# Performance work log

Hardware: AMD Instinct MI355X
Metric: run time of the kernel (lower is better)

## Reference

```python
import jax, jax.numpy as jnp
import numpy as np

NUM_HEADS = 16
HIDDEN = 1024
HEAD_DIM = HIDDEN // NUM_HEADS


def setup_inputs() -> dict:
    key = jax.random.key(0)
    ks = jax.random.split(key, 9)
    B, S = 2, 2048
    scale = 1.0 / np.sqrt(HIDDEN)
    x = jax.random.normal(ks[0], (B, S, HIDDEN), dtype=jnp.float32)
    Wq = jax.random.uniform(ks[1], (HIDDEN, HIDDEN), jnp.float32, -scale, scale)
    bq = jax.random.uniform(ks[2], (HIDDEN,), jnp.float32, -scale, scale)
    Wk = jax.random.uniform(ks[3], (HIDDEN, HIDDEN), jnp.float32, -scale, scale)
    bk = jax.random.uniform(ks[4], (HIDDEN,), jnp.float32, -scale, scale)
    Wv = jax.random.uniform(ks[5], (HIDDEN, HIDDEN), jnp.float32, -scale, scale)
    bv = jax.random.uniform(ks[6], (HIDDEN,), jnp.float32, -scale, scale)
    Wo = jax.random.uniform(ks[7], (HIDDEN, HIDDEN), jnp.float32, -scale, scale)
    bo = jax.random.uniform(ks[8], (HIDDEN,), jnp.float32, -scale, scale)
    return {"x": x, "Wq": Wq, "bq": bq, "Wk": Wk, "bk": bk,
            "Wv": Wv, "bv": bv, "Wo": Wo, "bo": bo}


def reference(x, Wq, bq, Wk, bk, Wv, bv, Wo, bo):
    B, S, _ = x.shape
    H, D = NUM_HEADS, HEAD_DIM
    # projections (torch Linear: x @ W^T + b)
    q = (x @ Wq.T + bq).reshape(B, S, H, D).transpose(0, 2, 1, 3)  # [B,H,S,D]
    k = (x @ Wk.T + bk).reshape(B, S, H, D).transpose(0, 2, 1, 3)
    v = (x @ Wv.T + bv).reshape(B, S, H, D).transpose(0, 2, 1, 3)
    scores = jnp.einsum("bhqd,bhkd->bhqk", q, k) / jnp.sqrt(jnp.float32(D))
    causal = jnp.tril(jnp.ones((S, S), dtype=bool))  # True = keep
    scores = jnp.where(causal, scores, -jnp.inf)
    weights = jax.nn.softmax(scores, axis=-1)
    out = jnp.einsum("bhqk,bhkd->bhqd", weights, v)  # [B,H,S,D]
    out = out.transpose(0, 2, 1, 3).reshape(B, S, H * D)
    return out @ Wo.T + bo
```

## Files before the change

### kernel.cpp

```cpp
#include <hip/hip_runtime.h>
#include <stdint.h>


#define HIDDEN 1024
#define NH 16
#define HD 64
#define BATCH 2
#define SEQ 2048

typedef unsigned short u16;
typedef unsigned int u32;
typedef __attribute__((ext_vector_type(8))) short short8;
typedef __attribute__((ext_vector_type(4))) float f32x4;

typedef const __attribute__((address_space(1))) u32 gu32;
typedef __attribute__((address_space(3))) u32 lu32;

__device__ __forceinline__ u16 f2bf(float f) {
    u32 u = __float_as_uint(f);
    return (u16)((u + 0x7FFFu + ((u >> 16) & 1u)) >> 16);
}

__global__ void cvt_all(const float* __restrict__ x, const float* __restrict__ Wq,
                        const float* __restrict__ Wk, const float* __restrict__ Wv,
                        const float* __restrict__ Wo, u16* __restrict__ xb,
                        u16* __restrict__ wqb, u16* __restrict__ wkb,
                        u16* __restrict__ wvb, u16* __restrict__ wob) {
    const int blk = blockIdx.x;
    const float* src; u16* dst; int base;
    if (blk < 2048)      { src = x;  dst = xb;  base = blk; }
    else if (blk < 2560) { src = Wq; dst = wqb; base = blk - 2048; }
    else if (blk < 3072) { src = Wk; dst = wkb; base = blk - 2560; }
    else if (blk < 3584) { src = Wv; dst = wvb; base = blk - 3072; }
    else                 { src = Wo; dst = wob; base = blk - 3584; }
    const int i = base * 256 + threadIdx.x;
    float4 a = ((const float4*)src)[2 * i];
    float4 b = ((const float4*)src)[2 * i + 1];
    union { u16 h[8]; uint4 v; } o;
    o.h[0] = f2bf(a.x); o.h[1] = f2bf(a.y); o.h[2] = f2bf(a.z); o.h[3] = f2bf(a.w);
    o.h[4] = f2bf(b.x); o.h[5] = f2bf(b.y); o.h[6] = f2bf(b.z); o.h[7] = f2bf(b.w);
    ((uint4*)dst)[i] = o.v;
}

#define GEMM_LDA 40
__device__ __forceinline__ void gemm_kloop(const u16* __restrict__ A,
                                           const u16* __restrict__ Wt,
                                           u16* As, u16* Bs, f32x4 (*acc)[4],
                                           int m0, int n0, int t) {
    const int lane = t & 63;
    const int w = t >> 6;
    const int quad = lane >> 4;
    const int lm = lane & 15;
    const int wm = (w & 1) * 64;
    const int wn = (w >> 1) * 64;
    const int srow = t >> 2;
    const int schunk = (t & 3) * 8;
    for (int k0 = 0; k0 < 1024; k0 += 32) {
        uint4 a0 = *(const uint4*)(A + (size_t)(m0 + srow) * 1024 + k0 + schunk);
        uint4 a1 = *(const uint4*)(A + (size_t)(m0 + srow + 64) * 1024 + k0 + schunk);
        uint4 b0 = *(const uint4*)(Wt + (size_t)(n0 + srow) * 1024 + k0 + schunk);
        uint4 b1 = *(const uint4*)(Wt + (size_t)(n0 + srow + 64) * 1024 + k0 + schunk);
        __syncthreads();
        *(uint4*)(As + srow * GEMM_LDA + schunk) = a0;
        *(uint4*)(As + (srow + 64) * GEMM_LDA + schunk) = a1;
        *(uint4*)(Bs + srow * GEMM_LDA + schunk) = b0;
        *(uint4*)(Bs + (srow + 64) * GEMM_LDA + schunk) = b1;
        __syncthreads();
        short8 af[4], bf[4];
#pragma unroll
        for (int mi = 0; mi < 4; mi++)
            af[mi] = *(const short8*)(As + (wm + mi * 16 + lm) * GEMM_LDA + quad * 8);
#pragma unroll
        for (int ni = 0; ni < 4; ni++)
            bf[ni] = *(const short8*)(Bs + (wn + ni * 16 + lm) * GEMM_LDA + quad * 8);
#pragma unroll
        for (int mi = 0; mi < 4; mi++)
#pragma unroll
            for (int ni = 0; ni < 4; ni++)
                acc[mi][ni] = __builtin_amdgcn_mfma_f32_16x16x32_bf16(
                    af[mi], bf[ni], acc[mi][ni], 0, 0, 0);
    }
}

__launch_bounds__(256, 2)
__global__ void gemm_qkv(const u16* __restrict__ A, const u16* __restrict__ Wqb,
                         const u16* __restrict__ Wkb, const u16* __restrict__ Wvb,
                         const float* __restrict__ bq, const float* __restrict__ bk,
                         const float* __restrict__ bv, u16* __restrict__ Qo,
                         u16* __restrict__ Ko, u16* __restrict__ Vo) {
    __shared__ u16 As[128 * GEMM_LDA];
    __shared__ u16 Bs[128 * GEMM_LDA];
    const int which = blockIdx.x >> 3;
    const int n0 = (blockIdx.x & 7) * 128;
    const int m0 = blockIdx.y * 128;
    const u16* Wt = (which == 0) ? Wqb : (which == 1) ? Wkb : Wvb;
    const float* bias = (which == 0) ? bq : (which == 1) ? bk : bv;
    u16* out = (which == 0) ? Qo : (which == 1) ? Ko : Vo;
    const float oscale = (which == 0) ? 0.18033688011112042f : 1.0f;
    const int t = threadIdx.x;
    const int lane = t & 63, w = t >> 6, quad = lane >> 4, lm = lane & 15;
    const int wm = (w & 1) * 64, wn = (w >> 1) * 64;

    f32x4 acc[4][4] = {};
    gemm_kloop(A, Wt, As, Bs, acc, m0, n0, t);

#pragma unroll
    for (int ni = 0; ni < 4; ni++) {
        const int n = n0 + wn + ni * 16 + lm;
        const float bv_ = bias[n];
        const int h = n >> 6, d = n & 63;
#pragma unroll
        for (int mi = 0; mi < 4; mi++)
#pragma unroll
            for (int r = 0; r < 4; r++) {
                const int m = m0 + wm + mi * 16 + quad * 4 + r;
                const int b = m >> 11, s = m & 2047;
                const u16 hv = f2bf((acc[mi][ni][r] + bv_) * oscale);
                if (which == 2)
                    out[(((size_t)(b * NH + h) * HD + d) * SEQ) + s] = hv;
                else
                    out[(((size_t)(b * NH + h) * SEQ + s) * HD) + d] = hv;
            }
    }
}

__launch_bounds__(256, 2)
__global__ void gemm_out(const u16* __restrict__ A, const u16* __restrict__ Wt,
                         const float* __restrict__ bias, float* __restrict__ out) {
    __shared__ u16 As[128 * GEMM_LDA];
    __shared__ u16 Bs[128 * GEMM_LDA];
    const int n0 = blockIdx.x * 128;
    const int m0 = blockIdx.y * 128;
    const int t = threadIdx.x;
    const int lane = t & 63, w = t >> 6, quad = lane >> 4, lm = lane & 15;
    const int wm = (w & 1) * 64, wn = (w >> 1) * 64;

    f32x4 acc[4][4] = {};
    gemm_kloop(A, Wt, As, Bs, acc, m0, n0, t);

#pragma unroll
    for (int ni = 0; ni < 4; ni++) {
        const int n = n0 + wn + ni * 16 + lm;
        const float bv_ = bias[n];
#pragma unroll
        for (int mi = 0; mi < 4; mi++)
#pragma unroll
            for (int r = 0; r < 4; r++) {
                const int m = m0 + wm + mi * 16 + quad * 4 + r;
                out[(size_t)m * 1024 + n] = acc[mi][ni][r] + bv_;
            }
    }
}

__launch_bounds__(256, 3)
__global__ void attn_kernel(const u16* __restrict__ Q, const u16* __restrict__ K,
                            const u16* __restrict__ Vt, u16* __restrict__ Out) {
    constexpr int LDP = 68;
    __shared__ u16 Ks[2][64 * 64];
    __shared__ u16 Vs[2][64 * 64];
    __shared__ u16 Ps[4 * 16 * LDP];
    const int t = threadIdx.x;
    const int lane = t & 63, w = t >> 6, quad = lane >> 4, lm = lane & 15;
    const int qt = 31 - (blockIdx.x >> 5);
    const int bh = blockIdx.x & 31;
    const int b = bh >> 4, h = bh & 15;
    const size_t base = (size_t)(b * NH + h) * SEQ * HD;
    const u16* Qg = Q + base;
    const u16* Kg = K + base;
    const u16* Vg = Vt + base;
    const int q0 = qt * 64 + w * 16;
    const int nk = qt + 1;

    short8 qf[2];
#pragma unroll
    for (int kk = 0; kk < 2; kk++)
        qf[kk] = *(const short8*)(Qg + (size_t)(q0 + lm) * HD + kk * 32 + quad * 8);

    f32x4 oacc[4] = {};
    f32x4 lacc = {};
    short8 ones;
#pragma unroll
    for (int j = 0; j < 8; j++) ones[j] = (short)0x3F80;

    u16* Pw = Ps + w * 16 * LDP;

    const int srow = (lane >> 3);
    const int schunk = (lane & 7) ^ srow;
    auto stage_kv = [&](int kt, int buf) {
#pragma unroll
        for (int j = 0; j < 2; j++) {
            const int row = w * 16 + j * 8 + srow;
            const u16* gk = Kg + (size_t)(kt * 64 + row) * HD + schunk * 8;
            const u16* gv = Vg + (size_t)row * SEQ + kt * 64 + schunk * 8;
            __builtin_amdgcn_global_load_lds((gu32*)gk, (lu32*)(&Ks[buf][(w * 16 + j * 8) * 64]), 16, 0, 0);
            __builtin_amdgcn_global_load_lds((gu32*)gv, (lu32*)(&Vs[buf][(w * 16 + j * 8) * 64]), 16, 0, 0);
        }
    };

    auto compute_step = [&](const u16* Kc, const u16* Vc, int kt_) {
        f32x4 sacc[4];
#pragma unroll
        for (int n = 0; n < 4; n++) {
            const int r = n * 16 + lm;
            const u16* rowp = Kc + r * 64;
            short8 kf0 = *(const short8*)(rowp + ((quad ^ (r & 7)) * 8));
            short8 kf1 = *(const short8*)(rowp + (((quad + 4) ^ (r & 7)) * 8));
            f32x4 a = {};
            a = __builtin_amdgcn_mfma_f32_16x16x32_bf16(qf[0], kf0, a, 0, 0, 0);
            a = __builtin_amdgcn_mfma_f32_16x16x32_bf16(qf[1], kf1, a, 0, 0, 0);
            sacc[n] = a;
        }
        if (kt_ == qt) {
#pragma unroll
            for (int n = 0; n < 4; n++)
#pragma unroll
                for (int r = 0; r < 4; r++)
                    if (n * 16 + lm > w * 16 + quad * 4 + r)
                        sacc[n][r] = -__builtin_inff();
        }
#pragma unroll
        for (int n = 0; n < 4; n++)
#pragma unroll
            for (int r = 0; r < 4; r++)
                Pw[(quad * 4 + r) * LDP + n * 16 + lm] =
                    (u16)(__float_as_uint(exp2f(sacc[n][r])) >> 16);
        short8 pf[2];
#pragma unroll
        for (int k4 = 0; k4 < 2; k4++)
            pf[k4] = *(const short8*)(Pw + lm * LDP + k4 * 32 + quad * 8);
#pragma unroll
        for (int n = 0; n < 4; n++) {
            const int r = n * 16 + lm;
            const u16* rowp = Vc + r * 64;
#pragma unroll
            for (int k4 = 0; k4 < 2; k4++) {
                short8 vf = *(const short8*)(rowp + (((k4 * 4 + quad) ^ (r & 7)) * 8));
                oacc[n] = __builtin_amdgcn_mfma_f32_16x16x32_bf16(pf[k4], vf, oacc[n], 0, 0, 0);
            }
        }
#pragma unroll
        for (int k4 = 0; k4 < 2; k4++)
            lacc = __builtin_amdgcn_mfma_f32_16x16x32_bf16(pf[k4], ones, lacc, 0, 0, 0);
    };

    stage_kv(0, 0);
    __syncthreads();

    for (int kt = 0; kt < nk; kt++) {
        const int cur = kt & 1;
        if (kt + 1 < nk) stage_kv(kt + 1, cur ^ 1);
        compute_step(Ks[cur], Vs[cur], kt);
        __syncthreads();
    }

    float inv[4];
#pragma unroll
    for (int r = 0; r < 4; r++) inv[r] = 1.0f / lacc[r];
#pragma unroll
    for (int n = 0; n < 4; n++)
#pragma unroll
        for (int r = 0; r < 4; r++) {
            const int qq = q0 + quad * 4 + r;
            Out[(size_t)(b * SEQ + qq) * HIDDEN + h * HD + n * 16 + lm] =
                f2bf(oacc[n][r] * inv[r]);
        }
}

extern "C" void kernel_launch(void* const* d_in, const int* in_sizes, int n_in,
                              void* d_out, int out_size, void* d_ws, size_t ws_size,
                              hipStream_t stream) {
    const float* x  = (const float*)d_in[0];
    const float* Wq = (const float*)d_in[1];
    const float* bq = (const float*)d_in[2];
    const float* Wk = (const float*)d_in[3];
    const float* bk = (const float*)d_in[4];
    const float* Wv = (const float*)d_in[5];
    const float* bv = (const float*)d_in[6];
    const float* Wo = (const float*)d_in[7];
    const float* bo = (const float*)d_in[8];
    float* out = (float*)d_out;

    char* ws = (char*)d_ws;
    const size_t SZ_X = (size_t)4096 * 1024 * 2;
    const size_t SZ_W = (size_t)1024 * 1024 * 2;
    u16* xb    = (u16*)(ws);
    u16* wqb   = (u16*)(ws + SZ_X);
    u16* wkb   = (u16*)(ws + SZ_X + SZ_W);
    u16* wvb   = (u16*)(ws + SZ_X + 2 * SZ_W);
    u16* wob   = (u16*)(ws + SZ_X + 3 * SZ_W);
    u16* Qb    = (u16*)(ws + SZ_X + 4 * SZ_W);
    u16* Kb    = (u16*)(ws + 2 * SZ_X + 4 * SZ_W);
    u16* Vtb   = (u16*)(ws + 3 * SZ_X + 4 * SZ_W);
    u16* attnb = (u16*)(ws + 4 * SZ_X + 4 * SZ_W);

    cvt_all<<<4096, 256, 0, stream>>>(x, Wq, Wk, Wv, Wo, xb, wqb, wkb, wvb, wob);
    gemm_qkv<<<dim3(24, 32), 256, 0, stream>>>(xb, wqb, wkb, wvb, bq, bk, bv, Qb, Kb, Vtb);
    attn_kernel<<<BATCH * NH * (SEQ / 64), 256, 0, stream>>>(Qb, Kb, Vtb, attnb);
    gemm_out<<<dim3(8, 32), 256, 0, stream>>>(attnb, wob, bo, out);
}
```

Before: 204.5 us.

## Double-buffer GEMM tiles via direct global-to-LDS loads with XOR swizzle

Both projection GEMMs now stage tiles with global_load_lds straight into double-buffered LDS, using an XOR swizzle in place of padding. This overlaps the next k-tile load with the current MFMAs and removes a sync per iteration. gemm_out also uses 64-row M tiles to double its block count and improve CU fill, and gemm_qkv's occupancy bound rises to 3. The changes add dependence on async LDS load ordering and the correctness of the swizzle.

```diff
diff --git a/kernel.cpp b/kernel.cpp
--- a/kernel.cpp
+++ b/kernel.cpp
@@ -42,54 +42,22 @@
     ((uint4*)dst)[i] = o.v;
 }
 
-#define GEMM_LDA 40
-__device__ __forceinline__ void gemm_kloop(const u16* __restrict__ A,
-                                           const u16* __restrict__ Wt,
-                                           u16* As, u16* Bs, f32x4 (*acc)[4],
-                                           int m0, int n0, int t) {
-    const int lane = t & 63;
-    const int w = t >> 6;
-    const int quad = lane >> 4;
-    const int lm = lane & 15;
-    const int wm = (w & 1) * 64;
-    const int wn = (w >> 1) * 64;
-    const int srow = t >> 2;
-    const int schunk = (t & 3) * 8;
-    for (int k0 = 0; k0 < 1024; k0 += 32) {
-        uint4 a0 = *(const uint4*)(A + (size_t)(m0 + srow) * 1024 + k0 + schunk);
-        uint4 a1 = *(const uint4*)(A + (size_t)(m0 + srow + 64) * 1024 + k0 + schunk);
-        uint4 b0 = *(const uint4*)(Wt + (size_t)(n0 + srow) * 1024 + k0 + schunk);
-        uint4 b1 = *(const uint4*)(Wt + (size_t)(n0 + srow + 64) * 1024 + k0 + schunk);
-        __syncthreads();
-        *(uint4*)(As + srow * GEMM_LDA + schunk) = a0;
-        *(uint4*)(As + (srow + 64) * GEMM_LDA + schunk) = a1;
-        *(uint4*)(Bs + srow * GEMM_LDA + schunk) = b0;
-        *(uint4*)(Bs + (srow + 64) * GEMM_LDA + schunk) = b1;
-        __syncthreads();
-        short8 af[4], bf[4];
-#pragma unroll
-        for (int mi = 0; mi < 4; mi++)
-            af[mi] = *(const short8*)(As + (wm + mi * 16 + lm) * GEMM_LDA + quad * 8);
-#pragma unroll
-        for (int ni = 0; ni < 4; ni++)
-            bf[ni] = *(const short8*)(Bs + (wn + ni * 16 + lm) * GEMM_LDA + quad * 8);
-#pragma unroll
-        for (int mi = 0; mi < 4; mi++)
-#pragma unroll
-            for (int ni = 0; ni < 4; ni++)
-                acc[mi][ni] = __builtin_amdgcn_mfma_f32_16x16x32_bf16(
-                    af[mi], bf[ni], acc[mi][ni], 0, 0, 0);
-    }
-}
-
-__launch_bounds__(256, 2)
+__device__ __forceinline__ void stage16(const u16* __restrict__ G, int grow0,
+                                        int k0, u16* lds, int rbase, int lane) {
+    const int sr = lane >> 2;
+    const int lc = (lane & 3) ^ (sr & 3);
+    const u16* g = G + (size_t)(grow0 + rbase + sr) * 1024 + k0 + lc * 8;
+    __builtin_amdgcn_global_load_lds((gu32*)g, (lu32*)(lds + rbase * 32), 16, 0, 0);
+}
+
+__launch_bounds__(256, 3)
 __global__ void gemm_qkv(const u16* __restrict__ A, const u16* __restrict__ Wqb,
                          const u16* __restrict__ Wkb, const u16* __restrict__ Wvb,
                          const float* __restrict__ bq, const float* __restrict__ bk,
                          const float* __restrict__ bv, u16* __restrict__ Qo,
                          u16* __restrict__ Ko, u16* __restrict__ Vo) {
-    __shared__ u16 As[128 * GEMM_LDA];
-    __shared__ u16 Bs[128 * GEMM_LDA];
+    __shared__ u16 As[2][128 * 32];
+    __shared__ u16 Bs[2][128 * 32];
     const int which = blockIdx.x >> 3;
     const int n0 = (blockIdx.x & 7) * 128;
     const int m0 = blockIdx.y * 128;
@@ -102,7 +70,35 @@
     const int wm = (w & 1) * 64, wn = (w >> 1) * 64;
 
     f32x4 acc[4][4] = {};
-    gemm_kloop(A, Wt, As, Bs, acc, m0, n0, t);
+
+    auto stage = [&](int k0, int buf) {
+        stage16(A, m0, k0, As[buf], w * 32, lane);
+        stage16(A, m0, k0, As[buf], w * 32 + 16, lane);
+        stage16(Wt, n0, k0, Bs[buf], w * 32, lane);
+        stage16(Wt, n0, k0, Bs[buf], w * 32 + 16, lane);
+    };
+
+    stage(0, 0);
+    __syncthreads();
+    for (int k0 = 0; k0 < 1024; k0 += 32) {
+        const int cur = (k0 >> 5) & 1;
+        if (k0 + 32 < 1024) stage(k0 + 32, cur ^ 1);
+        short8 af[4], bf[4];
+        const int sw = (quad ^ (lm & 3)) * 8;
+#pragma unroll
+        for (int mi = 0; mi < 4; mi++)
+            af[mi] = *(const short8*)(&As[cur][(wm + mi * 16 + lm) * 32] + sw);
+#pragma unroll
+        for (int ni = 0; ni < 4; ni++)
+            bf[ni] = *(const short8*)(&Bs[cur][(wn + ni * 16 + lm) * 32] + sw);
+#pragma unroll
+        for (int mi = 0; mi < 4; mi++)
+#pragma unroll
+            for (int ni = 0; ni < 4; ni++)
+                acc[mi][ni] = __builtin_amdgcn_mfma_f32_16x16x32_bf16(
+                    af[mi], bf[ni], acc[mi][ni], 0, 0, 0);
+        __syncthreads();
+    }
 
 #pragma unroll
     for (int ni = 0; ni < 4; ni++) {
@@ -127,23 +123,50 @@
 __launch_bounds__(256, 2)
 __global__ void gemm_out(const u16* __restrict__ A, const u16* __restrict__ Wt,
                          const float* __restrict__ bias, float* __restrict__ out) {
-    __shared__ u16 As[128 * GEMM_LDA];
-    __shared__ u16 Bs[128 * GEMM_LDA];
+    __shared__ u16 As[2][64 * 32];
+    __shared__ u16 Bs[2][128 * 32];
     const int n0 = blockIdx.x * 128;
-    const int m0 = blockIdx.y * 128;
+    const int m0 = blockIdx.y * 64;
     const int t = threadIdx.x;
     const int lane = t & 63, w = t >> 6, quad = lane >> 4, lm = lane & 15;
-    const int wm = (w & 1) * 64, wn = (w >> 1) * 64;
-
-    f32x4 acc[4][4] = {};
-    gemm_kloop(A, Wt, As, Bs, acc, m0, n0, t);
+    const int wm = (w & 1) * 32, wn = (w >> 1) * 64;
+
+    f32x4 acc[2][4] = {};
+
+    auto stage = [&](int k0, int buf) {
+        stage16(A, m0, k0, As[buf], w * 16, lane);
+        stage16(Wt, n0, k0, Bs[buf], w * 32, lane);
+        stage16(Wt, n0, k0, Bs[buf], w * 32 + 16, lane);
+    };
+
+    stage(0, 0);
+    __syncthreads();
+    for (int k0 = 0; k0 < 1024; k0 += 32) {
+        const int cur = (k0 >> 5) & 1;
+        if (k0 + 32 < 1024) stage(k0 + 32, cur ^ 1);
+        short8 af[2], bf[4];
+        const int sw = (quad ^ (lm & 3)) * 8;
+#pragma unroll
+        for (int mi = 0; mi < 2; mi++)
+            af[mi] = *(const short8*)(&As[cur][(wm + mi * 16 + lm) * 32] + sw);
+#pragma unroll
+        for (int ni = 0; ni < 4; ni++)
+            bf[ni] = *(const short8*)(&Bs[cur][(wn + ni * 16 + lm) * 32] + sw);
+#pragma unroll
+        for (int mi = 0; mi < 2; mi++)
+#pragma unroll
+            for (int ni = 0; ni < 4; ni++)
+                acc[mi][ni] = __builtin_amdgcn_mfma_f32_16x16x32_bf16(
+                    af[mi], bf[ni], acc[mi][ni], 0, 0, 0);
+        __syncthreads();
+    }
 
 #pragma unroll
     for (int ni = 0; ni < 4; ni++) {
         const int n = n0 + wn + ni * 16 + lm;
         const float bv_ = bias[n];
 #pragma unroll
-        for (int mi = 0; mi < 4; mi++)
+        for (int mi = 0; mi < 2; mi++)
 #pragma unroll
             for (int r = 0; r < 4; r++) {
                 const int m = m0 + wm + mi * 16 + quad * 4 + r;
@@ -296,5 +319,5 @@
     cvt_all<<<4096, 256, 0, stream>>>(x, Wq, Wk, Wv, Wo, xb, wqb, wkb, wvb, wob);
     gemm_qkv<<<dim3(24, 32), 256, 0, stream>>>(xb, wqb, wkb, wvb, bq, bk, bv, Qb, Kb, Vtb);
     attn_kernel<<<BATCH * NH * (SEQ / 64), 256, 0, stream>>>(Qb, Kb, Vtb, attnb);
-    gemm_out<<<dim3(8, 32), 256, 0, stream>>>(attnb, wob, bo, out);
-}
+    gemm_out<<<dim3(8, 64), 256, 0, stream>>>(attnb, wob, bo, out);
+}
```

Measured after the change: 200.6 us. About the same (-1.9%).
